# Performance work log

Hardware: AMD Instinct MI355X
Metric: run time of the kernel (lower is better)

Reference implementation:

```python
import jax, jax.numpy as jnp
import numpy as np

OUT, IN = 4096, 4096
GROUP_SIZE = 128
NUMEL = OUT * IN                 # 16,777,216 int4 values
N_GROUPS = NUMEL // GROUP_SIZE   # 131,072
N_PACKED = NUMEL // 2            # 8,388,608 bytes (stored as int32 0..255)


def _dequantize_int4(q_packed, q_scales, q_zeros):
    """Unpack two 4-bit values per byte, dequant per group, reshape to (OUT, IN)."""
    low = q_packed & 0xF                     # [N_PACKED]
    high = (q_packed >> 4) & 0xF             # [N_PACKED]
    # interleave: flat[2i] = low nibble, flat[2i+1] = high nibble
    q = jnp.stack([low, high], axis=-1).reshape(NUMEL)            # [NUMEL] int
    qg = q.astype(jnp.float32).reshape(N_GROUPS, GROUP_SIZE)      # [G, group]
    w = (qg - q_zeros[:, None]) * q_scales[:, None]
    return w.reshape(OUT, IN)


def setup_inputs() -> dict:
    key = jax.random.key(0)
    k = jax.random.split(key, 6)
    x = jax.random.normal(k[0], (4, 2048, IN), dtype=jnp.float32)
    q_packed = jax.random.randint(k[1], (N_PACKED,), 0, 256, dtype=jnp.int32)
    q_scales = jax.random.uniform(k[2], (N_GROUPS,), dtype=jnp.float32) * 0.02 + 1e-3
    q_zeros = jax.random.uniform(k[3], (N_GROUPS,), dtype=jnp.float32) * 15.0
    delta_weight = jax.random.normal(k[4], (OUT, IN), dtype=jnp.float32) * 0.01
    bias = jax.random.normal(k[5], (OUT,), dtype=jnp.float32)
    return {"x": x, "q_packed": q_packed, "q_scales": q_scales,
            "q_zeros": q_zeros, "delta_weight": delta_weight, "bias": bias}


def reference(x, q_packed, q_scales, q_zeros, delta_weight, bias):
    W = _dequantize_int4(q_packed, q_scales, q_zeros)   # [OUT, IN]
    W_eff = W + delta_weight
    # F.linear: y = x @ W_eff^T + bias
    h = jnp.einsum('bsi,oi->bso', x, W_eff) + bias
    return h
```

## Files before the change

### kernel.cpp

```cpp
#include <hip/hip_runtime.h>


#define M_DIM 8192
#define N_DIM 4096
#define K_DIM 4096
#define NUMEL (N_DIM * K_DIM)

typedef _Float16 half_t;
typedef __attribute__((ext_vector_type(4))) _Float16 half4v;
typedef __attribute__((ext_vector_type(8))) _Float16 half8v;
typedef __attribute__((ext_vector_type(4))) float float4v;
typedef __attribute__((ext_vector_type(4))) int int4v;

#define BM 128
#define BN 128
#define BK 64
#define KTILES (K_DIM / BK)
#define TILE_BYTES 16384
#define LDT 72

static __device__ __forceinline__ void gload16(const void* g, void* l) {
    __builtin_amdgcn_global_load_lds(
        (const __attribute__((address_space(1))) void*)g,
        (__attribute__((address_space(3))) void*)l, 16, 0, 0);
}

__global__ __launch_bounds__(256) void k_pack_w(
    const int* __restrict__ qp, const float* __restrict__ sc,
    const float* __restrict__ zr, const float* __restrict__ dwt,
    unsigned char* __restrict__ Wp)
{
    const long t = (long)blockIdx.x * 256 + threadIdx.x;
    const long flat = t * 8;
    const int g = (int)(flat >> 7);
    const float s = sc[g];
    const float zs = zr[g] * s;
    int4v q4 = *(const int4v*)(qp + (flat >> 1));
    float4v d0 = *(const float4v*)(dwt + flat);
    float4v d1 = *(const float4v*)(dwt + flat + 4);
    float d[8] = {d0[0], d0[1], d0[2], d0[3], d1[0], d1[1], d1[2], d1[3]};
    half8v vh;
#pragma unroll
    for (int j = 0; j < 4; ++j) {
        vh[2*j]   = (half_t)fmaf((float)(q4[j] & 15),        s, d[2*j]   - zs);
        vh[2*j+1] = (half_t)fmaf((float)((q4[j] >> 4) & 15), s, d[2*j+1] - zs);
    }
    const int n = (int)(flat >> 12);
    const int k = (int)(flat & 4095);
    const int row = n & 127;
    const int a = (row << 7) + ((k & 63) << 1);
    const int b = a ^ ((row & 7) << 4);
    *(half8v*)(Wp + (((size_t)((n >> 7) * KTILES + (k >> 6))) << 14) + b) = vh;
}

__global__ __launch_bounds__(256) void k_pack_x(
    const float* __restrict__ X, unsigned char* __restrict__ Xp)
{
    const long flat = ((long)blockIdx.x * 256 + threadIdx.x) * 8;
    float4v x0 = *(const float4v*)(X + flat);
    float4v x1 = *(const float4v*)(X + flat + 4);
    half8v vh;
    vh[0] = (half_t)x0[0]; vh[1] = (half_t)x0[1];
    vh[2] = (half_t)x0[2]; vh[3] = (half_t)x0[3];
    vh[4] = (half_t)x1[0]; vh[5] = (half_t)x1[1];
    vh[6] = (half_t)x1[2]; vh[7] = (half_t)x1[3];
    const int m = (int)(flat >> 12);
    const int k = (int)(flat & 4095);
    const int row = m & 127;
    const int a = (row << 7) + ((k & 63) << 1);
    const int b = a ^ ((row & 7) << 4);
    *(half8v*)(Xp + (((size_t)((m >> 7) * KTILES + (k >> 6))) << 14) + b) = vh;
}

template<int PACKED>
__global__ __launch_bounds__(256, 4) void k_gemm1(
    const unsigned char* __restrict__ Ap, const unsigned char* __restrict__ Bp,
    const float* __restrict__ X, const int* __restrict__ qp,
    const float* __restrict__ sc, const float* __restrict__ zr,
    const float* __restrict__ dwt,
    const float* __restrict__ bias, float* __restrict__ Y)
{
    __shared__ __align__(16) unsigned char smem[36864];

    const int tid  = threadIdx.x;
    const int lane = tid & 63;
    const int wave = tid >> 6;
    const int wm = wave >> 1, wn = wave & 1;
    const int bn = blockIdx.x & 31;
    const int bm = blockIdx.x >> 5;
    const long m0 = (long)bm * BM;
    const long n0 = (long)bn * BN;
    const int fr = lane & 15;

    const float4v zero4 = {0.f, 0.f, 0.f, 0.f};
    float4v acc[4][4];
#pragma unroll
    for (int i = 0; i < 4; ++i)
#pragma unroll
        for (int j = 0; j < 4; ++j) acc[i][j] = zero4;

    if constexpr (PACKED) {
        unsigned char* Ab = smem;
        unsigned char* Bb = smem + TILE_BYTES;
        const int kg16 = (lane >> 4) << 4;
        const unsigned char* at0 = Ap + (((size_t)bm * KTILES) << 14)
                                 + (wave << 12) + (lane << 4);
        const unsigned char* bt0 = Bp + (((size_t)bn * KTILES) << 14)
                                 + (wave << 12) + (lane << 4);
        for (int kb = 0; kb < KTILES; ++kb) {
            const unsigned char* at = at0 + ((size_t)kb << 14);
            const unsigned char* bt = bt0 + ((size_t)kb << 14);
#pragma unroll
            for (int i = 0; i < 4; ++i) {
                gload16(at + i * 1024, Ab + (wave << 12) + i * 1024);
                gload16(bt + i * 1024, Bb + (wave << 12) + i * 1024);
            }
            __syncthreads();
#pragma unroll
            for (int ks = 0; ks < 2; ++ks) {
                const int c2 = ks * 64 + kg16;
                half8v ah[4], bh[4];
#pragma unroll
                for (int i = 0; i < 4; ++i) {
                    const int ra = wm * 64 + i * 16 + fr;
                    ah[i] = *(const half8v*)(Ab + (((ra << 7) + c2) ^ ((ra & 7) << 4)));
                    const int rb = wn * 64 + i * 16 + fr;
                    bh[i] = *(const half8v*)(Bb + (((rb << 7) + c2) ^ ((rb & 7) << 4)));
                }
#pragma unroll
                for (int i = 0; i < 4; ++i)
#pragma unroll
                    for (int j = 0; j < 4; ++j)
                        acc[i][j] = __builtin_amdgcn_mfma_f32_16x16x32_f16(
                            ah[i], bh[j], acc[i][j], 0, 0, 0);
            }
            __syncthreads();
        }
    } else {
        half_t* Ah = (half_t*)smem;
        half_t* Bh = (half_t*)(smem + 2 * BM * LDT);
        const int ko = (lane >> 4) * 8;
        for (int k0 = 0; k0 < K_DIM; k0 += BK) {
            {
                const int ar = tid >> 4;
                const int ac = (tid & 15) * 4;
#pragma unroll
                for (int rr = 0; rr < 8; ++rr) {
                    const int row = ar + rr * 16;
                    float4v xv = *(const float4v*)(X + (m0 + row) * K_DIM + k0 + ac);
                    half4v h;
#pragma unroll
                    for (int j = 0; j < 4; ++j) h[j] = (half_t)xv[j];
                    *(half4v*)(Ah + row * LDT + ac) = h;
                }
            }
            {
                const int cr = tid >> 3;
                const int cc = (tid & 7) * 8;
#pragma unroll
                for (int rr = 0; rr < 4; ++rr) {
                    const int row = cr + rr * 32;
                    const long n = n0 + row;
                    const int g = (int)(n * 32 + (k0 >> 7));
                    const float s = sc[g];
                    const float zs = zr[g] * s;
                    const long flat = n * K_DIM + k0 + cc;
                    int4v q4 = *(const int4v*)(qp + (flat >> 1));
                    float4v d0 = *(const float4v*)(dwt + flat);
                    float4v d1 = *(const float4v*)(dwt + flat + 4);
                    float d[8] = {d0[0], d0[1], d0[2], d0[3], d1[0], d1[1], d1[2], d1[3]};
                    half8v vh;
#pragma unroll
                    for (int j = 0; j < 4; ++j) {
                        vh[2*j]   = (half_t)fmaf((float)(q4[j] & 15),        s, d[2*j]   - zs);
                        vh[2*j+1] = (half_t)fmaf((float)((q4[j] >> 4) & 15), s, d[2*j+1] - zs);
                    }
                    *(half8v*)(Bh + row * LDT + cc) = vh;
                }
            }
            __syncthreads();
#pragma unroll
            for (int ks = 0; ks < 2; ++ks) {
                const int kk = ks * 32 + ko;
                half8v ah[4], bh[4];
#pragma unroll
                for (int i = 0; i < 4; ++i) {
                    ah[i] = *(const half8v*)(Ah + (wm * 64 + i * 16 + fr) * LDT + kk);
                    bh[i] = *(const half8v*)(Bh + (wn * 64 + i * 16 + fr) * LDT + kk);
                }
#pragma unroll
                for (int i = 0; i < 4; ++i)
#pragma unroll
                    for (int j = 0; j < 4; ++j)
                        acc[i][j] = __builtin_amdgcn_mfma_f32_16x16x32_f16(
                            ah[i], bh[j], acc[i][j], 0, 0, 0);
            }
            __syncthreads();
        }
    }

#pragma unroll
    for (int i = 0; i < 4; ++i) {
        const long mrow = m0 + wm * 64 + i * 16 + (lane >> 4) * 4;
#pragma unroll
        for (int j = 0; j < 4; ++j) {
            const long col = n0 + wn * 64 + j * 16 + (lane & 15);
            const float b = bias[col];
#pragma unroll
            for (int r = 0; r < 4; ++r) {
                Y[(mrow + r) * N_DIM + col] = acc[i][j][r] + b;
            }
        }
    }
}

extern "C" void kernel_launch(void* const* d_in, const int* in_sizes, int n_in,
                              void* d_out, int out_size, void* d_ws, size_t ws_size,
                              hipStream_t stream)
{
    const float* X  = (const float*)d_in[0];
    const int*   qp = (const int*)d_in[1];
    const float* sc = (const float*)d_in[2];
    const float* zr = (const float*)d_in[3];
    const float* dwt = (const float*)d_in[4];
    const float* bs = (const float*)d_in[5];
    float* Y = (float*)d_out;

    const size_t needB = (size_t)N_DIM * K_DIM * 2;
    const size_t needA = (size_t)M_DIM * K_DIM * 2;

    dim3 blk(256);
    dim3 ggrid((M_DIM / BM) * (N_DIM / BN));

    if (ws_size >= needA + needB) {
        unsigned char* Bpk = (unsigned char*)d_ws;
        unsigned char* Apk = Bpk + needB;
        k_pack_w<<<dim3(NUMEL / 8 / 256), blk, 0, stream>>>(qp, sc, zr, dwt, Bpk);
        k_pack_x<<<dim3((M_DIM * K_DIM) / 8 / 256), blk, 0, stream>>>(X, Apk);
        k_gemm1<1><<<ggrid, blk, 0, stream>>>(Apk, Bpk, nullptr, nullptr, nullptr,
                                              nullptr, nullptr, bs, Y);
    } else {
        k_gemm1<0><<<ggrid, blk, 0, stream>>>(nullptr, nullptr, X, qp, sc, zr,
                                              dwt, bs, Y);
    }
}
```

Before: 315.1 us.

## Replace packed GEMM with 256x256 double-buffered 8-wave phased MFMA kernel

```diff
diff --git a/kernel.cpp b/kernel.cpp
--- a/kernel.cpp
+++ b/kernel.cpp
@@ -12,11 +12,7 @@
 typedef __attribute__((ext_vector_type(4))) float float4v;
 typedef __attribute__((ext_vector_type(4))) int int4v;
 
-#define BM 128
-#define BN 128
-#define BK 64
-#define KTILES (K_DIM / BK)
-#define TILE_BYTES 16384
+#define KTILES 64
 #define LDT 72
 
 static __device__ __forceinline__ void gload16(const void* g, void* l) {
@@ -72,15 +68,168 @@
     *(half8v*)(Xp + (((size_t)((m >> 7) * KTILES + (k >> 6))) << 14) + b) = vh;
 }
 
-template<int PACKED>
-__global__ __launch_bounds__(256, 4) void k_gemm1(
-    const unsigned char* __restrict__ Ap, const unsigned char* __restrict__ Bp,
+#define BARX() do { __builtin_amdgcn_sched_barrier(0); \
+                    __builtin_amdgcn_s_barrier(); \
+                    __builtin_amdgcn_sched_barrier(0); } while(0)
+#define WAITV(N) do { asm volatile("s_waitcnt vmcnt(" #N ")" ::: "memory"); \
+                      __builtin_amdgcn_sched_barrier(0); } while(0)
+
+#define READ_A(BUF, F0) do { \
+_Pragma("unroll") for (int i_ = 0; i_ < 4; ++i_) { \
+    const int row_ = ((F0) + i_) * 16 + fr; \
+_Pragma("unroll") for (int ks_ = 0; ks_ < 2; ++ks_) { \
+        const int off_ = ks_ * 64 + kg16; \
+        ah[i_][ks_] = *(const half8v*)(&lds[BUF][wm][row_ * 128 + (off_ ^ swz)]); \
+    } } } while(0)
+
+#define READ_B(BUF, DST, J0) do { \
+_Pragma("unroll") for (int j_ = 0; j_ < 2; ++j_) { \
+    const int row_ = bbase + ((J0) + j_) * 16 + fr; \
+_Pragma("unroll") for (int ks_ = 0; ks_ < 2; ++ks_) { \
+        const int off_ = ks_ * 64 + kg16; \
+        DST[j_][ks_] = *(const half8v*)(&lds[BUF][bhalf][row_ * 128 + (off_ ^ swz)]); \
+    } } } while(0)
+
+#define MFMA_Q(F0, N0, BREG) do { \
+    __builtin_amdgcn_s_setprio(1); \
+_Pragma("unroll") for (int i_ = 0; i_ < 4; ++i_) \
+_Pragma("unroll") for (int j_ = 0; j_ < 2; ++j_) \
+_Pragma("unroll") for (int ks_ = 0; ks_ < 2; ++ks_) \
+        acc[(F0)+i_][(N0)+j_] = __builtin_amdgcn_mfma_f32_16x16x32_f16( \
+            ah[i_][ks_], BREG[j_][ks_], acc[(F0)+i_][(N0)+j_], 0, 0, 0); \
+    __builtin_amdgcn_s_setprio(0); \
+} while(0)
+
+__global__ __launch_bounds__(512, 2) void k_gemm8ph(
+    const unsigned char* __restrict__ Apk, const unsigned char* __restrict__ Bpk,
+    const float* __restrict__ bias, float* __restrict__ Y)
+{
+    __shared__ __align__(16) unsigned char lds[2][4][16384];
+
+    const int tid  = threadIdx.x;
+    const int lane = tid & 63;
+    const int wave = tid >> 6;
+    const int wm = wave >> 2;
+    const int wn = wave & 3;
+    const int bhalf = 2 + (wn >> 1);
+    const int bbase = (wn & 1) * 64;
+    const int fr   = lane & 15;
+    const int kg16 = (lane >> 4) << 4;
+    const int swz  = (fr & 7) << 4;
+
+    const int wg = blockIdx.x;
+    const int swg = (wg & 7) * 64 + (wg >> 3);
+    const int bn = swg & 15;
+    const int bm = swg >> 4;
+
+    auto asrc = [&](int h, int tk) {
+        return Apk + ((((size_t)(2 * bm + h)) * KTILES + tk) << 14);
+    };
+    auto bsrc = [&](int h, int tk) {
+        return Bpk + ((((size_t)(2 * bn + h)) * KTILES + tk) << 14);
+    };
+    auto stageh = [&](int b, int h, const unsigned char* s) {
+        unsigned char* d = &lds[b][h][tid << 4];
+        gload16(s + (tid << 4), d);
+        gload16(s + 8192 + (tid << 4), d + 8192);
+    };
+
+    half8v ah[4][2], b01[2][2], b23[2][2];
+    float4v acc[8][4];
+    const float4v zero4 = {0.f, 0.f, 0.f, 0.f};
+#pragma unroll
+    for (int i = 0; i < 8; ++i)
+#pragma unroll
+        for (int j = 0; j < 4; ++j) acc[i][j] = zero4;
+
+    stageh(0, 0, asrc(0, 0)); stageh(0, 1, asrc(1, 0));
+    stageh(0, 2, bsrc(0, 0)); stageh(0, 3, bsrc(1, 0));
+    stageh(1, 0, asrc(0, 1)); stageh(1, 1, asrc(1, 1));
+    WAITV(4);
+    BARX();
+
+    for (int it = 0; it < 31; ++it) {
+        const int t1 = 2 * it + 1, t2 = 2 * it + 2, t3 = 2 * it + 3;
+        READ_A(0, 0); READ_B(0, b01, 0);
+        stageh(1, 2, bsrc(0, t1)); stageh(1, 3, bsrc(1, t1));
+        BARX();
+        MFMA_Q(0, 0, b01);
+        BARX();
+        READ_B(0, b23, 2);
+        BARX();
+        MFMA_Q(0, 2, b23);
+        BARX();
+        READ_A(0, 4);
+        BARX();
+        MFMA_Q(4, 2, b23);
+        BARX();
+        stageh(0, 0, asrc(0, t2)); stageh(0, 1, asrc(1, t2));
+        BARX();
+        MFMA_Q(4, 0, b01);
+        WAITV(4);
+        BARX();
+        READ_A(1, 0); READ_B(1, b01, 0);
+        stageh(0, 2, bsrc(0, t2)); stageh(0, 3, bsrc(1, t2));
+        BARX();
+        MFMA_Q(0, 0, b01);
+        BARX();
+        READ_B(1, b23, 2);
+        BARX();
+        MFMA_Q(0, 2, b23);
+        BARX();
+        READ_A(1, 4);
+        BARX();
+        MFMA_Q(4, 2, b23);
+        BARX();
+        stageh(1, 0, asrc(0, t3)); stageh(1, 1, asrc(1, t3));
+        BARX();
+        MFMA_Q(4, 0, b01);
+        WAITV(4);
+        BARX();
+    }
+
+    READ_A(0, 0); READ_B(0, b01, 0);
+    stageh(1, 2, bsrc(0, 63)); stageh(1, 3, bsrc(1, 63));
+    BARX(); MFMA_Q(0, 0, b01); BARX();
+    READ_B(0, b23, 2);
+    BARX(); MFMA_Q(0, 2, b23); BARX();
+    READ_A(0, 4);
+    BARX(); MFMA_Q(4, 2, b23); BARX();
+    BARX(); MFMA_Q(4, 0, b01);
+    WAITV(0);
+    BARX();
+    READ_A(1, 0); READ_B(1, b01, 0);
+    BARX(); MFMA_Q(0, 0, b01); BARX();
+    READ_B(1, b23, 2);
+    BARX(); MFMA_Q(0, 2, b23); BARX();
+    READ_A(1, 4);
+    BARX(); MFMA_Q(4, 2, b23); BARX();
+    BARX(); MFMA_Q(4, 0, b01); BARX();
+
+    const long m0 = (long)bm * 256 + wm * 128;
+    const long n0 = (long)bn * 256 + wn * 64;
+#pragma unroll
+    for (int mf = 0; mf < 8; ++mf) {
+        const long row = m0 + mf * 16 + (lane >> 4) * 4;
+#pragma unroll
+        for (int nf = 0; nf < 4; ++nf) {
+            const long col = n0 + nf * 16 + (lane & 15);
+            const float b = bias[col];
+#pragma unroll
+            for (int r = 0; r < 4; ++r)
+                Y[(row + r) * N_DIM + col] = acc[mf][nf][r] + b;
+        }
+    }
+}
+
+__global__ __launch_bounds__(256, 2) void k_gemm_fused(
     const float* __restrict__ X, const int* __restrict__ qp,
     const float* __restrict__ sc, const float* __restrict__ zr,
     const float* __restrict__ dwt,
     const float* __restrict__ bias, float* __restrict__ Y)
 {
-    __shared__ __align__(16) unsigned char smem[36864];
+    __shared__ __align__(16) half_t Ah[128 * LDT];
+    __shared__ __align__(16) half_t Bh[128 * LDT];
 
     const int tid  = threadIdx.x;
     const int lane = tid & 63;
@@ -88,9 +237,10 @@
     const int wm = wave >> 1, wn = wave & 1;
     const int bn = blockIdx.x & 31;
     const int bm = blockIdx.x >> 5;
-    const long m0 = (long)bm * BM;
-    const long n0 = (long)bn * BN;
+    const long m0 = (long)bm * 128;
+    const long n0 = (long)bn * 128;
     const int fr = lane & 15;
+    const int ko = (lane >> 4) * 8;
 
     const float4v zero4 = {0.f, 0.f, 0.f, 0.f};
     float4v acc[4][4];
@@ -99,104 +249,62 @@
 #pragma unroll
         for (int j = 0; j < 4; ++j) acc[i][j] = zero4;
 
-    if constexpr (PACKED) {
-        unsigned char* Ab = smem;
-        unsigned char* Bb = smem + TILE_BYTES;
-        const int kg16 = (lane >> 4) << 4;
-        const unsigned char* at0 = Ap + (((size_t)bm * KTILES) << 14)
-                                 + (wave << 12) + (lane << 4);
-        const unsigned char* bt0 = Bp + (((size_t)bn * KTILES) << 14)
-                                 + (wave << 12) + (lane << 4);
-        for (int kb = 0; kb < KTILES; ++kb) {
-            const unsigned char* at = at0 + ((size_t)kb << 14);
-            const unsigned char* bt = bt0 + ((size_t)kb << 14);
+    for (int k0 = 0; k0 < K_DIM; k0 += 64) {
+        {
+            const int ar = tid >> 4;
+            const int ac = (tid & 15) * 4;
+#pragma unroll
+            for (int rr = 0; rr < 8; ++rr) {
+                const int row = ar + rr * 16;
+                float4v xv = *(const float4v*)(X + (m0 + row) * K_DIM + k0 + ac);
+                half4v h;
+#pragma unroll
+                for (int j = 0; j < 4; ++j) h[j] = (half_t)xv[j];
+                *(half4v*)(Ah + row * LDT + ac) = h;
+            }
+        }
+        {
+            const int cr = tid >> 3;
+            const int cc = (tid & 7) * 8;
+#pragma unroll
+            for (int rr = 0; rr < 4; ++rr) {
+                const int row = cr + rr * 32;
+                const long n = n0 + row;
+                const int g = (int)(n * 32 + (k0 >> 7));
+                const float s = sc[g];
+                const float zs = zr[g] * s;
+                const long flat = n * K_DIM + k0 + cc;
+                int4v q4 = *(const int4v*)(qp + (flat >> 1));
+                float4v d0 = *(const float4v*)(dwt + flat);
+                float4v d1 = *(const float4v*)(dwt + flat + 4);
+                float d[8] = {d0[0], d0[1], d0[2], d0[3], d1[0], d1[1], d1[2], d1[3]};
+                half8v vh;
+#pragma unroll
+                for (int j = 0; j < 4; ++j) {
+                    vh[2*j]   = (half_t)fmaf((float)(q4[j] & 15),        s, d[2*j]   - zs);
+                    vh[2*j+1] = (half_t)fmaf((float)((q4[j] >> 4) & 15), s, d[2*j+1] - zs);
+                }
+                *(half8v*)(Bh + row * LDT + cc) = vh;
+            }
+        }
+        __syncthreads();
+#pragma unroll
+        for (int ks = 0; ks < 2; ++ks) {
+            const int kk = ks * 32 + ko;
+            half8v a2[4], b2[4];
 #pragma unroll
             for (int i = 0; i < 4; ++i) {
-                gload16(at + i * 1024, Ab + (wave << 12) + i * 1024);
-                gload16(bt + i * 1024, Bb + (wave << 12) + i * 1024);
+                a2[i] = *(const half8v*)(Ah + (wm * 64 + i * 16 + fr) * LDT + kk);
+                b2[i] = *(const half8v*)(Bh + (wn * 64 + i * 16 + fr) * LDT + kk);
             }
-            __syncthreads();
-#pragma unroll
-            for (int ks = 0; ks < 2; ++ks) {
-                const int c2 = ks * 64 + kg16;
-                half8v ah[4], bh[4];
-#pragma unroll
-                for (int i = 0; i < 4; ++i) {
-                    const int ra = wm * 64 + i * 16 + fr;
-                    ah[i] = *(const half8v*)(Ab + (((ra << 7) + c2) ^ ((ra & 7) << 4)));
-                    const int rb = wn * 64 + i * 16 + fr;
-                    bh[i] = *(const half8v*)(Bb + (((rb << 7) + c2) ^ ((rb & 7) << 4)));
-                }
-#pragma unroll
-                for (int i = 0; i < 4; ++i)
-#pragma unroll
-                    for (int j = 0; j < 4; ++j)
-                        acc[i][j] = __builtin_amdgcn_mfma_f32_16x16x32_f16(
-                            ah[i], bh[j], acc[i][j], 0, 0, 0);
-            }
-            __syncthreads();
-        }
-    } else {
-        half_t* Ah = (half_t*)smem;
-        half_t* Bh = (half_t*)(smem + 2 * BM * LDT);
-        const int ko = (lane >> 4) * 8;
-        for (int k0 = 0; k0 < K_DIM; k0 += BK) {
-            {
-                const int ar = tid >> 4;
-                const int ac = (tid & 15) * 4;
-#pragma unroll
-                for (int rr = 0; rr < 8; ++rr) {
-                    const int row = ar + rr * 16;
-                    float4v xv = *(const float4v*)(X + (m0 + row) * K_DIM + k0 + ac);
-                    half4v h;
-#pragma unroll
-                    for (int j = 0; j < 4; ++j) h[j] = (half_t)xv[j];
-                    *(half4v*)(Ah + row * LDT + ac) = h;
-                }
-            }
-            {
-                const int cr = tid >> 3;
-                const int cc = (tid & 7) * 8;
-#pragma unroll
-                for (int rr = 0; rr < 4; ++rr) {
-                    const int row = cr + rr * 32;
-                    const long n = n0 + row;
-                    const int g = (int)(n * 32 + (k0 >> 7));
-                    const float s = sc[g];
-                    const float zs = zr[g] * s;
-                    const long flat = n * K_DIM + k0 + cc;
-                    int4v q4 = *(const int4v*)(qp + (flat >> 1));
-                    float4v d0 = *(const float4v*)(dwt + flat);
-                    float4v d1 = *(const float4v*)(dwt + flat + 4);
-                    float d[8] = {d0[0], d0[1], d0[2], d0[3], d1[0], d1[1], d1[2], d1[3]};
-                    half8v vh;
-#pragma unroll
-                    for (int j = 0; j < 4; ++j) {
-                        vh[2*j]   = (half_t)fmaf((float)(q4[j] & 15),        s, d[2*j]   - zs);
-                        vh[2*j+1] = (half_t)fmaf((float)((q4[j] >> 4) & 15), s, d[2*j+1] - zs);
-                    }
-                    *(half8v*)(Bh + row * LDT + cc) = vh;
-                }
-            }
-            __syncthreads();
-#pragma unroll
-            for (int ks = 0; ks < 2; ++ks) {
-                const int kk = ks * 32 + ko;
-                half8v ah[4], bh[4];
-#pragma unroll
-                for (int i = 0; i < 4; ++i) {
-                    ah[i] = *(const half8v*)(Ah + (wm * 64 + i * 16 + fr) * LDT + kk);
-                    bh[i] = *(const half8v*)(Bh + (wn * 64 + i * 16 + fr) * LDT + kk);
-                }
-#pragma unroll
-                for (int i = 0; i < 4; ++i)
-#pragma unroll
-                    for (int j = 0; j < 4; ++j)
-                        acc[i][j] = __builtin_amdgcn_mfma_f32_16x16x32_f16(
-                            ah[i], bh[j], acc[i][j], 0, 0, 0);
-            }
-            __syncthreads();
-        }
+#pragma unroll
+            for (int i = 0; i < 4; ++i)
+#pragma unroll
+                for (int j = 0; j < 4; ++j)
+                    acc[i][j] = __builtin_amdgcn_mfma_f32_16x16x32_f16(
+                        a2[i], b2[j], acc[i][j], 0, 0, 0);
+        }
+        __syncthreads();
     }
 
 #pragma unroll
@@ -207,9 +315,8 @@
             const long col = n0 + wn * 64 + j * 16 + (lane & 15);
             const float b = bias[col];
 #pragma unroll
-            for (int r = 0; r < 4; ++r) {
+            for (int r = 0; r < 4; ++r)
                 Y[(mrow + r) * N_DIM + col] = acc[i][j][r] + b;
-            }
         }
     }
 }
@@ -229,18 +336,14 @@
     const size_t needB = (size_t)N_DIM * K_DIM * 2;
     const size_t needA = (size_t)M_DIM * K_DIM * 2;
 
-    dim3 blk(256);
-    dim3 ggrid((M_DIM / BM) * (N_DIM / BN));
-
     if (ws_size >= needA + needB) {
         unsigned char* Bpk = (unsigned char*)d_ws;
         unsigned char* Apk = Bpk + needB;
-        k_pack_w<<<dim3(NUMEL / 8 / 256), blk, 0, stream>>>(qp, sc, zr, dwt, Bpk);
-        k_pack_x<<<dim3((M_DIM * K_DIM) / 8 / 256), blk, 0, stream>>>(X, Apk);
-        k_gemm1<1><<<ggrid, blk, 0, stream>>>(Apk, Bpk, nullptr, nullptr, nullptr,
-                                              nullptr, nullptr, bs, Y);
+        k_pack_w<<<dim3(NUMEL / 8 / 256), dim3(256), 0, stream>>>(qp, sc, zr, dwt, Bpk);
+        k_pack_x<<<dim3((M_DIM * (size_t)K_DIM) / 8 / 256), dim3(256), 0, stream>>>(X, Apk);
+        k_gemm8ph<<<dim3((M_DIM / 256) * (N_DIM / 256)), dim3(512), 0, stream>>>(Apk, Bpk, bs, Y);
     } else {
-        k_gemm1<0><<<ggrid, blk, 0, stream>>>(nullptr, nullptr, X, qp, sc, zr,
-                                              dwt, bs, Y);
-    }
-}
+        k_gemm_fused<<<dim3((M_DIM / 128) * (N_DIM / 128)), dim3(256), 0, stream>>>(
+            X, qp, sc, zr, dwt, bs, Y);
+    }
+}
```

After: 297.0 us. 1.06x faster.
